# Kernel tuning notes

Hardware: AMD Instinct MI355X
Metric: run time of the kernel (lower is better)

## Reference

```python
import jax, jax.numpy as jnp
import numpy as np
from jax import lax
from jax.scipy.linalg import cho_solve, solve_triangular

N_MC, S, O, T, B, M, HL = 16, 4, 3, 128, 256, 32, 64
PAR = S * S + S + S * S  # 36 variational params per timestep
JIT = 1e-5
LOG2PI = float(np.log(2.0 * np.pi))


def _rbf(x, z, inv_ls, os_d):
    # x [..., D], z [M, D] -> [..., M]
    d = (x[..., None, :] - z) * inv_ls
    return os_d * jnp.exp(-0.5 * jnp.sum(d * d, -1))


def setup_inputs():
    key = jax.random.key(0)
    ks = jax.random.split(key, 16)
    r = jax.random.normal
    obs = r(ks[0], (B, T, O), jnp.float32)
    Z = r(ks[1], (S, M, S), jnp.float32)
    log_ls = jnp.zeros((S, S), jnp.float32)
    log_os = jnp.zeros((S,), jnp.float32)
    m_u = 0.1 * r(ks[2], (S, M), jnp.float32)
    L_u = 0.1 * jnp.broadcast_to(jnp.eye(M, dtype=jnp.float32), (S, M, M)) \
        + 0.01 * jnp.tril(r(ks[3], (S, M, M), jnp.float32))
    noise_proc = 0.0025 * jnp.ones((S,), jnp.float32)  # process_noise_sd**2
    noise_emis = 0.01 * jnp.ones((O,), jnp.float32)    # emission_noise_sd**2
    def lin(k, o, i):
        return r(k, (o, i), jnp.float32) / np.sqrt(i).astype(np.float32)
    Wih = lin(ks[4], 4 * HL, O); Whh = lin(ks[5], 4 * HL, HL)
    b_lstm = jnp.zeros((4 * HL,), jnp.float32)
    Wm = lin(ks[6], S, HL); bm = jnp.zeros((S,), jnp.float32)
    Wv = lin(ks[7], S, HL); bv = jnp.zeros((S,), jnp.float32)
    W1 = lin(ks[8], 256, O); b1 = jnp.zeros((256,), jnp.float32)
    W2 = lin(ks[9], 128, 256); b2 = jnp.zeros((128,), jnp.float32)
    W3 = lin(ks[10], 64, 128); b3 = jnp.zeros((64,), jnp.float32)
    W4 = lin(ks[11], PAR, 64); b4 = jnp.zeros((PAR,), jnp.float32)
    return dict(obs=obs, Z=Z, log_ls=log_ls, log_os=log_os, m_u=m_u, L_u=L_u,
                noise_proc=noise_proc, noise_emis=noise_emis,
                Wih=Wih, Whh=Whh, b_lstm=b_lstm, Wm=Wm, bm=bm, Wv=Wv, bv=bv,
                W1=W1, b1=b1, W2=W2, b2=b2, W3=W3, b3=b3, W4=W4, b4=b4)


def reference(obs, Z, log_ls, log_os, m_u, L_u, noise_proc, noise_emis,
              Wih, Whh, b_lstm, Wm, bm, Wv, bv,
              W1, b1, W2, b2, W3, b3, W4, b4):
    ls = jnp.exp(log_ls)                  # [S, S] ARD lengthscales per GP output dim
    os_ = jnp.exp(log_os)                 # [S] outputscales
    inv_ls = 1.0 / ls
    H = jnp.eye(S, dtype=obs.dtype)[:O]   # fixed emission matrix (learn_emission=False)

    # ---- RecNet: LSTM over observations -> q(x0) = N(m0, diag(v0)) ----
    def lstm_cell(carry, x_t):
        h, c = carry
        g = x_t @ Wih.T + h @ Whh.T + b_lstm
        i, f, gg, o = jnp.split(g, 4, -1)
        c = jax.nn.sigmoid(f) * c + jax.nn.sigmoid(i) * jnp.tanh(gg)
        h = jax.nn.sigmoid(o) * jnp.tanh(c)
        return (h, c), None
    h0 = jnp.zeros((B, HL), obs.dtype)
    (hT, _), _ = lax.scan(lstm_cell, (h0, h0), obs.transpose(1, 0, 2))
    m0 = hT @ Wm.T + bm
    v0 = jax.nn.softplus(hT @ Wv.T + bv) + 1e-6
    # KL[q(x0) || N(0, I)]
    qm0_KL = jnp.mean(0.5 * jnp.sum(v0 + m0 ** 2 - 1.0 - jnp.log(v0), -1))

    # ---- sample x0 and inducing outputs U ~ q(u) (consistent sampling) ----
    rng = jax.random.key(42)
    k0, kU, kq = jax.random.split(rng, 3)
    eps0 = jax.random.normal(k0, (N_MC, S, B, S), obs.dtype)
    x_prev = m0 + jnp.sqrt(v0) * eps0     # [N_MC, S, B, S]
    Lu = jnp.tril(L_u)                    # [S, M, M]
    epsU = jax.random.normal(kU, (N_MC, S, M), obs.dtype)
    U = m_u + jnp.einsum('smk,nsk->nsm', Lu, epsU)  # [N_MC, S, M]

    # ---- per-output-dim GP precomputation ----
    Kzz = jax.vmap(lambda z, il, o: _rbf(z, z, il, o))(Z, inv_ls, os_) \
        + JIT * jnp.eye(M, dtype=obs.dtype)
    Lzz = jnp.linalg.cholesky(Kzz)        # [S, M, M]

    def cond_dim(Z_d, inv_ls_d, os_d, Lz_d, U_d, x_d):
        # condition GP dim d on sampled U_d: x_d [N,B,S], U_d [N,M]
        Kxz = _rbf(x_d, Z_d, inv_ls_d, os_d)              # [N,B,M]
        v = cho_solve((Lz_d, True), U_d.T).T              # Kzz^{-1} U, [N,M]
        mean = jnp.einsum('nbm,nm->nb', Kxz, v)
        W_ = cho_solve((Lz_d, True), Kxz.reshape(-1, M).T).T.reshape(N_MC, B, M)
        var = os_d - jnp.sum(Kxz * W_, -1)
        return mean, jnp.maximum(var, 1e-8)
    gp_cond = jax.vmap(cond_dim, in_axes=(0, 0, 0, 0, 1, 1))

    # ---- amortized inference net (4-layer MLP) for all timesteps ----
    h = jax.nn.relu(obs @ W1.T + b1)
    h = jax.nn.relu(h @ W2.T + b2)
    h = jax.nn.relu(h @ W3.T + b3)
    par = h @ W4.T + b4                    # [B, T, PAR]

    eps_q = jax.random.normal(kq, (T, N_MC, B, S), obs.dtype)
    eyeS = jnp.eye(S, dtype=obs.dtype)

    def step(carry, inp):
        x_p, KLa, lika = carry
        par_t, y_t, eps_t = inp            # [B,PAR], [B,O], [N,B,S]
        mean_d, var_d = gp_cond(Z, inv_ls, os_, Lzz, U, x_p)
        gpMean = mean_d.transpose(1, 2, 0)  # [N,B,S]
        gpVar = var_d.transpose(1, 2, 0)
        At = par_t[:, :S * S].reshape(B, S, S)
        bt = par_t[:, S * S:S * S + S]
        Stl = jnp.tril(par_t[:, S * S + S:].reshape(B, S, S))
        St = Stl @ Stl.transpose(0, 2, 1)
        q_mean = jnp.einsum('bij,nbj->nbi', At, gpMean) + bt          # [N,B,S]
        q_cov = St + jnp.einsum('bij,nbj,bkj->nbik', At, gpVar, At)   # [N,B,S,S]
        Lq = jnp.linalg.cholesky(q_cov + 1e-6 * eyeS)
        logdet_q = 2.0 * jnp.sum(jnp.log(jnp.diagonal(Lq, axis1=-2, axis2=-1)), -1)
        d0 = gpVar + noise_proc             # p(xt|ft) diag covariance
        kl_t = 0.5 * (jnp.sum(jnp.diagonal(q_cov, axis1=-2, axis2=-1) / d0, -1)
                      + jnp.sum((gpMean - q_mean) ** 2 / d0, -1)
                      - S + jnp.sum(jnp.log(d0), -1) - logdet_q)
        mu_y = q_mean @ H.T                 # [N,B,O]
        var_y = jnp.einsum('oi,nbij,oj->nbo', H, q_cov, H)
        ell = -0.5 * (LOG2PI + jnp.log(noise_emis)
                      + ((y_t - mu_y) ** 2 + var_y) / noise_emis)
        x_new = q_mean + jnp.einsum('nbij,nbj->nbi', Lq, eps_t)
        x_p = jnp.broadcast_to(x_new[:, None], (N_MC, S, B, S))
        return (x_p, KLa + jnp.mean(kl_t), lika + jnp.mean(jnp.sum(ell, -1))), None

    z0 = jnp.asarray(0.0, obs.dtype)
    (x_p, KL, lik), _ = lax.scan(step, (x_prev, z0, z0),
                                 (par.transpose(1, 0, 2), obs.transpose(1, 0, 2), eps_q))

    # ---- KL[q(u) || p(u)] of the variational GP ----
    A = solve_triangular(Lzz, Lu, lower=True)
    bq = solve_triangular(Lzz, m_u[..., None], lower=True)[..., 0]
    logdetK = 2.0 * jnp.sum(jnp.log(jnp.diagonal(Lzz, axis1=-2, axis2=-1)), -1)
    logdetS = 2.0 * jnp.sum(jnp.log(jnp.abs(jnp.diagonal(Lu, axis1=-2, axis2=-1)) + 1e-12), -1)
    gpKL = 0.5 * jnp.sum(jnp.sum(A ** 2, (-2, -1)) + jnp.sum(bq ** 2, -1)
                         - M + logdetK - logdetS) / (T * B)

    ELBO = -qm0_KL - gpKL + lik - KL
    ELBO = jnp.where(lik > KL, -qm0_KL - gpKL + lik / T - KL, ELBO)
    return ELBO
```

## Files before the change

kernel.cpp:

```cpp
#include <hip/hip_runtime.h>
#include <cstdint>
#include <math.h>

#define NMC   16
#define SDIM  4
#define ODIM  3
#define TLEN  128
#define BDIM  256
#define MDIM  32
#define HLDIM 64
#define PARD  36

#define LOG2PI_F 1.8378770664093453f

typedef float v2f __attribute__((ext_vector_type(2)));
__device__ __forceinline__ v2f v2(float x, float y) { v2f r; r.x = x; r.y = y; return r; }
__device__ __forceinline__ v2f v2s(float x) { return v2(x, x); }
#define PKFMA(a, b, c) __builtin_elementwise_fma((a), (b), (c))

__host__ __device__ inline void threefry2x32(uint32_t k0, uint32_t k1,
                                             uint32_t x0, uint32_t x1,
                                             uint32_t* o0, uint32_t* o1) {
  uint32_t ks0 = k0, ks1 = k1, ks2 = k0 ^ k1 ^ 0x1BD11BDAu;
  x0 += ks0; x1 += ks1;
#define TF_R(r) { x0 += x1; x1 = (x1 << (r)) | (x1 >> (32 - (r))); x1 ^= x0; }
  TF_R(13) TF_R(15) TF_R(26) TF_R(6)  x0 += ks1; x1 += ks2 + 1u;
  TF_R(17) TF_R(29) TF_R(16) TF_R(24) x0 += ks2; x1 += ks0 + 2u;
  TF_R(13) TF_R(15) TF_R(26) TF_R(6)  x0 += ks0; x1 += ks1 + 3u;
  TF_R(17) TF_R(29) TF_R(16) TF_R(24) x0 += ks1; x1 += ks2 + 4u;
  TF_R(13) TF_R(15) TF_R(26) TF_R(6)  x0 += ks2; x1 += ks0 + 5u;
#undef TF_R
  *o0 = x0; *o1 = x1;
}

__device__ inline float erfinv_f32(float x) {
  float w = -log1pf(-x * x);
  float p;
  if (w < 5.0f) {
    w -= 2.5f;
    p = 2.81022636e-08f;
    p = fmaf(p, w, 3.43273939e-07f);
    p = fmaf(p, w, -3.5233877e-06f);
    p = fmaf(p, w, -4.39150654e-06f);
    p = fmaf(p, w, 0.00021858087f);
    p = fmaf(p, w, -0.00125372503f);
    p = fmaf(p, w, -0.00417768164f);
    p = fmaf(p, w, 0.246640727f);
    p = fmaf(p, w, 1.50140941f);
  } else {
    w = sqrtf(w) - 3.0f;
    p = -0.000200214257f;
    p = fmaf(p, w, 0.000100950558f);
    p = fmaf(p, w, 0.00134934322f);
    p = fmaf(p, w, -0.00367342844f);
    p = fmaf(p, w, 0.00573950773f);
    p = fmaf(p, w, -0.0076224613f);
    p = fmaf(p, w, 0.00943887047f);
    p = fmaf(p, w, 1.00167406f);
    p = fmaf(p, w, 2.83297682f);
  }
  return p * x;
}

__device__ inline float bits_to_normal(uint32_t b) {
  float f = __uint_as_float((b >> 9) | 0x3F800000u) - 1.0f;
  const float lo = -0.99999994f;
  float u = f * 2.0f + lo;
  u = fmaxf(lo, u);
  return 1.41421356f * erfinv_f32(u);
}

#define DPP_ROR_ADD(v, ctrl) \
  ((v) + __int_as_float(__builtin_amdgcn_update_dpp(0, __float_as_int(v), (ctrl), 0xf, 0xf, false)))

__device__ __forceinline__ float allred32(float v) {
  v = DPP_ROR_ADD(v, 0x128);
  v = DPP_ROR_ADD(v, 0x124);
  v = DPP_ROR_ADD(v, 0x122);
  v = DPP_ROR_ADD(v, 0x121);
  return v + __shfl_xor(v, 16);
}

__device__ __forceinline__ float sigm_fast(float x) {
  return 1.0f / (1.0f + __expf(-x));
}
__device__ __forceinline__ float tanh_fast(float x) {
  return 1.0f - 2.0f / (1.0f + __expf(2.0f * x));
}


#define MLP_SB 128
__device__ void mlp_part(
    float* smem, const float* __restrict__ obs,
    const float* __restrict__ W1, const float* __restrict__ b1,
    const float* __restrict__ W2, const float* __restrict__ b2,
    const float* __restrict__ W3, const float* __restrict__ b3,
    const float* __restrict__ W4, const float* __restrict__ b4,
    float* __restrict__ par_g) {
  float* xs  = smem;
  float* A_l = smem + 192;
  float* B_l = smem + 192 + 4096;
  const int tid = threadIdx.x;
  const int R0 = blockIdx.x * 64;
  const int tr = tid & 15;
  const int tj = tid >> 4;

  for (int idx = tid; idx < 192; idx += 256) {
    int r = idx & 63, o = idx >> 6;
    xs[o * 64 + r] = obs[(R0 + r) * 3 + o];
  }

  float acc2[4][8];
#pragma unroll
  for (int i = 0; i < 4; ++i)
#pragma unroll
    for (int j = 0; j < 8; ++j) acc2[i][j] = 0.f;

  for (int kc = 0; kc < 4; ++kc) {
    __syncthreads();
    {
      int j = tid & 127, kh = (tid >> 7) * 32;
      const float4* wsrc = (const float4*)(W2 + j * 256 + kc * 64 + kh);
#pragma unroll
      for (int q = 0; q < 8; ++q) {
        float4 v = wsrc[q];
        int k = kh + q * 4;
        B_l[(k + 0) * MLP_SB + j] = v.x;
        B_l[(k + 1) * MLP_SB + j] = v.y;
        B_l[(k + 2) * MLP_SB + j] = v.z;
        B_l[(k + 3) * MLP_SB + j] = v.w;
      }
    }
    {
      int r = tid & 63, q4 = tid >> 6;
      float x0 = xs[r], x1 = xs[64 + r], x2 = xs[128 + r];
      const float4* w1p = (const float4*)(W1 + (kc * 64 + q4 * 16) * 3);
      float4 wv[12];
#pragma unroll
      for (int q = 0; q < 12; ++q) wv[q] = w1p[q];
      const float* wf = (const float*)wv;
#pragma unroll
      for (int i = 0; i < 16; ++i) {
        int k = q4 * 16 + i;
        float v = b1[kc * 64 + k] + wf[i * 3] * x0 + wf[i * 3 + 1] * x1 + wf[i * 3 + 2] * x2;
        A_l[k * 64 + r] = fmaxf(v, 0.f);
      }
    }
    __syncthreads();
    for (int k = 0; k < 64; ++k) {
      float4 av = *(const float4*)&A_l[k * 64 + tr * 4];
      float4 b0 = *(const float4*)&B_l[k * MLP_SB + tj * 8];
      float4 b1v = *(const float4*)&B_l[k * MLP_SB + tj * 8 + 4];
      const float a4[4] = {av.x, av.y, av.z, av.w};
      const float bv8[8] = {b0.x, b0.y, b0.z, b0.w, b1v.x, b1v.y, b1v.z, b1v.w};
#pragma unroll
      for (int ri = 0; ri < 4; ++ri)
#pragma unroll
        for (int ji = 0; ji < 8; ++ji)
          acc2[ri][ji] = fmaf(a4[ri], bv8[ji], acc2[ri][ji]);
    }
  }
  __syncthreads();
#pragma unroll
  for (int ji = 0; ji < 8; ++ji) {
    int j = tj * 8 + ji;
    float bias = b2[j];
    float4 hv;
    hv.x = fmaxf(acc2[0][ji] + bias, 0.f);
    hv.y = fmaxf(acc2[1][ji] + bias, 0.f);
    hv.z = fmaxf(acc2[2][ji] + bias, 0.f);
    hv.w = fmaxf(acc2[3][ji] + bias, 0.f);
    *(float4*)&B_l[j * 64 + tr * 4] = hv;
  }

  float acc3[4][4];
#pragma unroll
  for (int i = 0; i < 4; ++i)
#pragma unroll
    for (int j = 0; j < 4; ++j) acc3[i][j] = 0.f;

  for (int kc = 0; kc < 2; ++kc) {
    __syncthreads();
    {
      int j = tid & 63, kq = (tid >> 6) * 16;
      const float4* wsrc = (const float4*)(W3 + j * 128 + kc * 64 + kq);
#pragma unroll
      for (int q = 0; q < 4; ++q) {
        float4 v = wsrc[q];
        int k = kq + q * 4;
        A_l[(k + 0) * 64 + j] = v.x;
        A_l[(k + 1) * 64 + j] = v.y;
        A_l[(k + 2) * 64 + j] = v.z;
        A_l[(k + 3) * 64 + j] = v.w;
      }
    }
    __syncthreads();
    for (int k = 0; k < 64; ++k) {
      float4 av = *(const float4*)&B_l[(kc * 64 + k) * 64 + tr * 4];
      float4 bv = *(const float4*)&A_l[k * 64 + (tj & 15) * 4];
      const float a4[4] = {av.x, av.y, av.z, av.w};
      const float b4v[4] = {bv.x, bv.y, bv.z, bv.w};
#pragma unroll
      for (int ri = 0; ri < 4; ++ri)
#pragma unroll
        for (int ji = 0; ji < 4; ++ji)
          acc3[ri][ji] = fmaf(a4[ri], b4v[ji], acc3[ri][ji]);
    }
  }
  __syncthreads();
#pragma unroll
  for (int ji = 0; ji < 4; ++ji) {
    int j = tj * 4 + ji;
    float bias = b3[j];
    float4 hv;
    hv.x = fmaxf(acc3[0][ji] + bias, 0.f);
    hv.y = fmaxf(acc3[1][ji] + bias, 0.f);
    hv.z = fmaxf(acc3[2][ji] + bias, 0.f);
    hv.w = fmaxf(acc3[3][ji] + bias, 0.f);
    *(float4*)&A_l[j * 64 + tr * 4] = hv;
  }
  __syncthreads();

  {
    int r = tid & 63;
    int jg = __builtin_amdgcn_readfirstlane(tid >> 6);
    float accp[9];
#pragma unroll
    for (int i = 0; i < 9; ++i) accp[i] = b4[jg * 9 + i];
    for (int k = 0; k < 64; ++k) {
      float hv = A_l[k * 64 + r];
#pragma unroll
      for (int i = 0; i < 9; ++i)
        accp[i] = fmaf(hv, W4[(jg * 9 + i) * 64 + k], accp[i]);
    }
#pragma unroll
    for (int i = 0; i < 9; ++i) par_g[(R0 + r) * 36 + jg * 9 + i] = accp[i];
  }
}

__device__ void lstm_part(
    float* smem, int b, const float* __restrict__ obs,
    const float* __restrict__ Wih, const float* __restrict__ Whh,
    const float* __restrict__ b_lstm,
    const float* __restrict__ Wm, const float* __restrict__ bm,
    const float* __restrict__ Wv, const float* __restrict__ bv,
    float* __restrict__ m0_g, float* __restrict__ v0_g, float* __restrict__ acc) {
  float* g_l = smem;
  float* h_w = smem + 512;
  float* mv_l = smem + 768;
  float* obl = smem + 776;
  const int tid = threadIdx.x;
  const int w = tid >> 6;
  const int l = tid & 63;

  for (int i = tid; i < 384; i += 256) obl[(i / 3) * 4 + (i % 3)] = obs[b * 384 + i];

  float whh_r[64];
  {
    const float4* wsrc = (const float4*)(Whh + tid * 64);
#pragma unroll
    for (int q = 0; q < 16; ++q) {
      float4 v = wsrc[q];
      whh_r[q * 4 + 0] = v.x; whh_r[q * 4 + 1] = v.y;
      whh_r[q * 4 + 2] = v.z; whh_r[q * 4 + 3] = v.w;
    }
  }
  const float wih0 = Wih[tid * 3 + 0];
  const float wih1 = Wih[tid * 3 + 1];
  const float wih2 = Wih[tid * 3 + 2];
  const float bb = b_lstm[tid];

  float c_ = 0.0f;
  h_w[w * 64 + l] = 0.0f;
  __syncthreads();

#pragma unroll 1
  for (int t = 0; t < TLEN; ++t) {
    const float4 xv = *(const float4*)&obl[t * 4];
    const float4* h4 = (const float4*)&h_w[w * 64];
    float a0 = 0.f, a1 = 0.f, a2 = 0.f, a3 = 0.f;
#pragma unroll
    for (int q = 0; q < 16; ++q) {
      float4 hv = h4[q];
      a0 = fmaf(whh_r[q * 4 + 0], hv.x, a0);
      a1 = fmaf(whh_r[q * 4 + 1], hv.y, a1);
      a2 = fmaf(whh_r[q * 4 + 2], hv.z, a2);
      a3 = fmaf(whh_r[q * 4 + 3], hv.w, a3);
    }
    float g = fmaf(wih0, xv.x, fmaf(wih1, xv.y, fmaf(wih2, xv.z, bb))) + ((a0 + a1) + (a2 + a3));
    g_l[((t & 1) * 4 + w) * 64 + l] = g;
    __syncthreads();
    float gi = g_l[((t & 1) * 4 + 0) * 64 + l];
    float gf = g_l[((t & 1) * 4 + 1) * 64 + l];
    float gg = g_l[((t & 1) * 4 + 2) * 64 + l];
    float go = g_l[((t & 1) * 4 + 3) * 64 + l];
    c_ = sigm_fast(gf) * c_ + sigm_fast(gi) * tanh_fast(gg);
    h_w[w * 64 + l] = sigm_fast(go) * tanh_fast(c_);
  }

  if (tid < 8) {
    const int s = tid & 3;
    const bool isv = tid >= 4;
    const float* W = isv ? (Wv + s * 64) : (Wm + s * 64);
    float a = isv ? bv[s] : bm[s];
#pragma unroll
    for (int k = 0; k < 64; ++k) a += W[k] * h_w[k];
    if (!isv) {
      m0_g[b * 4 + s] = a;
      mv_l[s] = a;
    } else {
      float sp = (a > 0.f) ? (a + log1pf(expf(-a))) : log1pf(expf(a));
      float v = sp + 1e-6f;
      v0_g[b * 4 + s] = v;
      mv_l[4 + s] = v;
    }
  }
  if (tid == 0) {
    float s = 0.f;
#pragma unroll
    for (int k = 0; k < 4; ++k) {
      float m = mv_l[k], v = mv_l[4 + k];
      s += 0.5f * (v + m * m - 1.0f - logf(v));
    }
    atomicAdd(&acc[0], s);
  }
}

__device__ void setup_part(
    float* smem, int d, const float* __restrict__ Z,
    const float* __restrict__ log_ls, const float* __restrict__ log_os,
    const float* __restrict__ m_u, const float* __restrict__ L_u,
    uint32_t kUa, uint32_t kUb,
    float* __restrict__ Kinv_g, float* __restrict__ alpha_g, float* __restrict__ acc) {
  float* Kl    = smem;
  float* work  = smem + 1056;
  float* Ul    = smem + 2112;
  float* red   = smem + 2624;
  float* epsUl = smem + 2688;
  const int tid = threadIdx.x;

  {
    int nn7 = tid >> 5, k = tid & 31;
    uint32_t j = (uint32_t)((nn7 * 4 + d) * 32 + k);
    uint32_t o0, o1;
    threefry2x32(kUa, kUb, j, j + 1024u, &o0, &o1);
    epsUl[nn7 * 32 + k] = bits_to_normal(o0);
    epsUl[(nn7 + 8) * 32 + k] = bits_to_normal(o1);
  }

  float il[4];
#pragma unroll
  for (int k = 0; k < 4; ++k) il[k] = expf(-log_ls[d * 4 + k]);
  const float osd = expf(log_os[d]);

  for (int e = tid; e < 1024; e += 256) {
    int i = e >> 5, j = e & 31;
    float s = 0.f;
#pragma unroll
    for (int k = 0; k < 4; ++k) {
      float t_ = (Z[d * 128 + i * 4 + k] - Z[d * 128 + j * 4 + k]) * il[k];
      s += t_ * t_;
    }
    float v = osd * expf(-0.5f * s);
    if (i == j) v += 1e-5f;
    Kl[i * 33 + j] = v;
  }
  __syncthreads();

  for (int jc = 0; jc < 32; ++jc) {
    if (tid == jc) {
      float s = Kl[jc * 33 + jc];
      for (int p = 0; p < jc; ++p) s -= Kl[jc * 33 + p] * Kl[jc * 33 + p];
      Kl[jc * 33 + jc] = sqrtf(s);
    }
    __syncthreads();
    if (tid > jc && tid < 32) {
      float s = Kl[tid * 33 + jc];
      for (int p = 0; p < jc; ++p) s -= Kl[tid * 33 + p] * Kl[jc * 33 + p];
      Kl[tid * 33 + jc] = s / Kl[jc * 33 + jc];
    }
    __syncthreads();
  }

  if (tid < 32) {
    const int col = tid;
    float rdiag[32];
#pragma unroll
    for (int r = 0; r < 32; ++r) rdiag[r] = __builtin_amdgcn_rcpf(Kl[r * 33 + r]);
    float w[32];
#pragma unroll
    for (int r = 0; r < 32; ++r) {
      float s = (r == col) ? 1.f : 0.f;
#pragma unroll
      for (int p = 0; p < 32; ++p)
        if (p < r) s -= Kl[r * 33 + p] * w[p];
      w[r] = s * rdiag[r];
    }
    float w2[32];
#pragma unroll
    for (int rr = 0; rr < 32; ++rr) {
      const int r = 31 - rr;
      float s = w[r];
#pragma unroll
      for (int p = 0; p < 32; ++p)
        if (p > r) s -= Kl[p * 33 + r] * w2[p];
      w2[r] = s * rdiag[r];
    }
#pragma unroll
    for (int r = 0; r < 32; ++r) {
      Kinv_g[(((d >> 1) * 32 + r) * 32 + col) * 2 + (d & 1)] = w2[r];
      work[col * 33 + r] = w2[r];
    }
  }
  for (int e = tid; e < 512; e += 256) {
    int nn = e >> 5, m = e & 31;
    float s = m_u[d * 32 + m];
    for (int k = 0; k <= m; ++k)
      s += L_u[(d * 32 + m) * 32 + k] * epsUl[nn * 32 + k];
    Ul[nn * 32 + m] = s;
  }
  __syncthreads();
  for (int e = tid; e < 512; e += 256) {
    int nn = e >> 5, m = e & 31;
    float s = 0.f;
    for (int mm = 0; mm < 32; ++mm) s += work[mm * 33 + m] * Ul[nn * 32 + mm];
    alpha_g[(d * 16 + nn) * 32 + m] = s;
  }

  float contrib = 0.f;
  if (tid < 32) {
    const int col = tid;
    float rdiag[32];
#pragma unroll
    for (int r = 0; r < 32; ++r) rdiag[r] = __builtin_amdgcn_rcpf(Kl[r * 33 + r]);
    float v[32];
    float sa = 0.f;
#pragma unroll
    for (int r = 0; r < 32; ++r) {
      float lu = L_u[(d * 32 + r) * 32 + col];
      float s = (col <= r) ? lu : 0.f;
#pragma unroll
      for (int p = 0; p < 32; ++p)
        if (p < r) s -= Kl[r * 33 + p] * v[p];
      float vv = s * rdiag[r];
      v[r] = vv;
      sa += vv * vv;
    }
    contrib = sa;
  } else if (tid < 64) {
    float bq[32];
    float sb = 0.f;
#pragma unroll
    for (int r = 0; r < 32; ++r) {
      float s = m_u[d * 32 + r];
#pragma unroll
      for (int p = 0; p < 32; ++p)
        if (p < r) s -= Kl[r * 33 + p] * bq[p];
      float vv = s * __builtin_amdgcn_rcpf(Kl[r * 33 + r]);
      bq[r] = vv;
      sb += vv * vv;
    }
    contrib = (tid == 32) ? sb : 0.f;
  }
  if (tid < 64) red[tid] = contrib;
  __syncthreads();
  if (tid == 0) {
    float s = 0.f;
    for (int i = 0; i < 64; ++i) s += red[i];
    float ldK = 0.f, ldS = 0.f;
    for (int r = 0; r < 32; ++r) {
      ldK += logf(Kl[r * 33 + r]);
      ldS += logf(fabsf(L_u[(d * 32 + r) * 32 + r]) + 1e-12f);
    }
    float g = s - 32.0f + 2.0f * ldK - 2.0f * ldS;
    atomicAdd(&acc[1], 0.5f * g / (128.0f * 256.0f));
  }
}

__global__ __launch_bounds__(256) void prep_kernel(
    const float* obs,
    const float* W1, const float* b1, const float* W2, const float* b2,
    const float* W3, const float* b3, const float* W4, const float* b4,
    const float* Wih, const float* Whh, const float* b_lstm,
    const float* Wm, const float* bm, const float* Wv, const float* bv,
    const float* Z, const float* log_ls, const float* log_os,
    const float* m_u, const float* L_u,
    uint32_t kUa, uint32_t kUb,
    float* par_g, float* m0_g, float* v0_g,
    float* Kinv_g, float* alpha_g, float* acc) {
  __shared__ __align__(16) float smem[12480];
  const int bx = blockIdx.x;
  if (bx < 512) {
    mlp_part(smem, obs, W1, b1, W2, b2, W3, b3, W4, b4, par_g);
  } else if (bx < 768) {
    lstm_part(smem, bx - 512, obs, Wih, Whh, b_lstm, Wm, bm, Wv, bv, m0_g, v0_g, acc);
  } else {
    setup_part(smem, bx - 768, Z, log_ls, log_os, m_u, L_u, kUa, kUb,
               Kinv_g, alpha_g, acc);
  }
}

__global__ __launch_bounds__(256)
__attribute__((amdgpu_waves_per_eu(1, 2)))
void scan_kernel(
    const float* __restrict__ Z, const float* __restrict__ log_ls,
    const float* __restrict__ log_os, const float* __restrict__ noise_proc,
    const float* __restrict__ noise_emis, const float* __restrict__ obs,
    const float* __restrict__ par_g, const float* __restrict__ m0_g,
    const float* __restrict__ v0_g,
    const float* __restrict__ Kinv_g, const float* __restrict__ alpha_g,
    uint32_t k0a, uint32_t k0b, uint32_t kqa, uint32_t kqb,
    float* __restrict__ acc, float* __restrict__ out) {
  __shared__ __align__(16) float parl_raw[32 * 36];
  __shared__ __align__(16) float parl_pk[32 * 40];
  __shared__ __align__(16) float obsl[32 * 4];
  __shared__ __align__(16) float eps0l[8 * 4 * 4];
  __shared__ __align__(16) v2f kbufv[8][2][32];
  __shared__ __align__(16) float epsl[128 * 8 * 4];
  const int tid = threadIdx.x;
  const int c = tid >> 5;
  const int m = tid & 31;
  const int h = c & 1;
  const int cp = c & ~1;
  const int b = blockIdx.x >> 1;
  const int nb = (blockIdx.x & 1) << 3;
  const bool hh = (h != 0);

#pragma unroll
  for (int i = 0; i < 8; ++i) {
    int e = tid + 256 * i;
    int t = e >> 5, cc = (e >> 2) & 7, ss = e & 3;
    uint32_t j = (uint32_t)(((t * 16 + nb + cc) * 256 + b) * 4 + ss);
    uint32_t o0, o1;
    threefry2x32(kqa, kqb, j, j + 1048576u, &o0, &o1);
    epsl[e] = bits_to_normal(o0);
    epsl[((t + 64) * 8 + cc) * 4 + ss] = bits_to_normal(o1);
  }
  if (tid < 128) {
    int cc = tid >> 4, dd = (tid >> 2) & 3, ss = tid & 3;
    uint32_t j = (uint32_t)((((cc * 4 + dd) * 256 + b) * 4) + ss);
    uint32_t o0, o1;
    threefry2x32(k0a, k0b, j, j + 32768u, &o0, &o1);
    eps0l[(cc * 4 + dd) * 4 + ss] = bits_to_normal(nb ? o1 : o0);
  }

  v2f ilp[4], nzp[4], osp;
#pragma unroll
  for (int k = 0; k < 4; ++k) {
    float i0 = expf(-log_ls[(2 * h + 0) * 4 + k]);
    float i1 = expf(-log_ls[(2 * h + 1) * 4 + k]);
    ilp[k] = v2(i0, i1);
    nzp[k] = v2(-Z[(2 * h + 0) * 128 + m * 4 + k] * i0,
                -Z[(2 * h + 1) * 128 + m * 4 + k] * i1);
  }
  osp = v2(expf(log_os[2 * h + 0]), expf(log_os[2 * h + 1]));

  v2f kinv2[32];
  {
    const float4* kg4 = (const float4*)Kinv_g;
#pragma unroll
    for (int q = 0; q < 16; ++q) {
      float4 v = kg4[(h * 32 + m) * 16 + q];
      kinv2[2 * q + 0] = v2(v.x, v.y);
      kinv2[2 * q + 1] = v2(v.z, v.w);
    }
  }
  v2f alrp[2];
#pragma unroll
  for (int cc = 0; cc < 2; ++cc)
    alrp[cc] = v2(alpha_g[((2 * h + 0) * 16 + nb + cp + cc) * 32 + m],
                  alpha_g[((2 * h + 1) * 16 + nb + cp + cc) * 32 + m]);
  float np_[4];
#pragma unroll
  for (int k = 0; k < 4; ++k) np_[k] = noise_proc[k];
  const float ine0 = __builtin_amdgcn_rcpf(noise_emis[0]);
  const float ine1 = __builtin_amdgcn_rcpf(noise_emis[1]);
  const float ine2 = __builtin_amdgcn_rcpf(noise_emis[2]);
  const float cst = 3.0f * LOG2PI_F + logf(noise_emis[0]) + logf(noise_emis[1]) + logf(noise_emis[2]);

  const float4 m0v = *(const float4*)(m0_g + b * 4);
  const float4 v0v = *(const float4*)(v0_g + b * 4);
  const float sq0 = sqrtf(v0v.x), sq1 = sqrtf(v0v.y), sq2 = sqrtf(v0v.z), sq3 = sqrtf(v0v.w);

  __syncthreads();
  v2f kt0[2];
#pragma unroll
  for (int cc = 0; cc < 2; ++cc) {
    const float4 ea = *(const float4*)&eps0l[((cp + cc) * 4 + 2 * h + 0) * 4];
    const float4 eb = *(const float4*)&eps0l[((cp + cc) * 4 + 2 * h + 1) * 4];
    v2f xt0p = v2(fmaf(sq0, ea.x, m0v.x), fmaf(sq0, eb.x, m0v.x));
    v2f xt1p = v2(fmaf(sq1, ea.y, m0v.y), fmaf(sq1, eb.y, m0v.y));
    v2f xt2p = v2(fmaf(sq2, ea.z, m0v.z), fmaf(sq2, eb.z, m0v.z));
    v2f xt3p = v2(fmaf(sq3, ea.w, m0v.w), fmaf(sq3, eb.w, m0v.w));
    v2f d0 = PKFMA(xt0p, ilp[0], nzp[0]);
    v2f d1 = PKFMA(xt1p, ilp[1], nzp[1]);
    v2f d2 = PKFMA(xt2p, ilp[2], nzp[2]);
    v2f d3 = PKFMA(xt3p, ilp[3], nzp[3]);
    v2f ss = PKFMA(d0, d0, PKFMA(d1, d1, PKFMA(d2, d2, d3 * d3)));
    v2f km = osp * v2(__expf(-0.5f * ss.x), __expf(-0.5f * ss.y));
    kt0[cc] = km;
    kbufv[cp + cc][h][m] = km;
  }

  float x0r = 0.f, x1r = 0.f, x2r = 0.f, x3r = 0.f;
  float kl_acc = 0.f, ell_acc = 0.f;

  for (int tc = 0; tc < 4; ++tc) {
    __syncthreads();
    {
      const float4* src = (const float4*)(par_g + (size_t)b * 4608 + tc * 1152);
      float4* dst = (float4*)parl_raw;
      for (int i = tid; i < 288; i += 256) dst[i] = src[i];
      if (tid < 96) obsl[(tid / 3) * 4 + (tid % 3)] = obs[b * 384 + tc * 96 + tid];
    }
    __syncthreads();
    {
      int st = tid >> 3, w = tid & 7;
      const float* r = parl_raw + st * 36;
      float* o = parl_pk + st * 40;
      if (w < 4) {
        o[2 * w + 0] = r[0 * 4 + w]; o[2 * w + 1] = r[1 * 4 + w];
        o[8 + 2 * w + 0] = r[2 * 4 + w]; o[8 + 2 * w + 1] = r[3 * 4 + w];
      } else if (w == 4) {
        o[16] = r[16]; o[17] = r[17]; o[18] = r[18]; o[19] = r[19];
      } else if (w == 5) {
        float l00 = r[20];
        o[20] = l00 * l00;
        o[21] = r[24] * l00;
        o[22] = r[28] * l00;
        o[23] = r[32] * l00;
      } else if (w == 6) {
        o[24] = r[28] * r[24] + r[29] * r[25];
        o[25] = r[32] * r[24] + r[33] * r[25];
        o[28] = r[24] * r[24] + r[25] * r[25];
      } else {
        o[26] = r[28] * r[28] + r[29] * r[29] + r[30] * r[30];
        o[27] = r[32] * r[28] + r[33] * r[29] + r[34] * r[30];
        o[29] = r[32] * r[32] + r[33] * r[33] + r[34] * r[34] + r[35] * r[35];
      }
    }
    __syncthreads();

#pragma unroll 1
    for (int tt = 0; tt < 32; ++tt) {
      const int t = tc * 32 + tt;
      const v2f* pk = (const v2f*)&parl_pk[tt * 40];
      v2f Ac01[4], Ac23[4];
#pragma unroll
      for (int k = 0; k < 4; ++k) { Ac01[k] = pk[k]; Ac23[k] = pk[4 + k]; }
      const v2f bt01 = pk[8], bt23 = pk[9];
      const v2f StA = pk[10];
      const v2f StB = pk[11];
      const v2f StD = pk[12];
      const v2f StE = pk[13];
      const v2f Stx = pk[14];
      const float4 ov = *(const float4*)&obsl[tt * 4];
      const float4 ev = *(const float4*)&epsl[(t * 8 + c) * 4];

      v2f kregp[2];
      if (t != 0) {
        const float xo0 = __shfl_xor(x0r, 32);
        const float xo1 = __shfl_xor(x1r, 32);
        const float xo2 = __shfl_xor(x2r, 32);
        const float xo3 = __shfl_xor(x3r, 32);
#pragma unroll
        for (int cc = 0; cc < 2; ++cc) {
          const bool own = (cc == h);
          float xt0 = own ? x0r : xo0;
          float xt1 = own ? x1r : xo1;
          float xt2 = own ? x2r : xo2;
          float xt3 = own ? x3r : xo3;
          v2f d0 = PKFMA(v2s(xt0), ilp[0], nzp[0]);
          v2f d1 = PKFMA(v2s(xt1), ilp[1], nzp[1]);
          v2f d2 = PKFMA(v2s(xt2), ilp[2], nzp[2]);
          v2f d3 = PKFMA(v2s(xt3), ilp[3], nzp[3]);
          v2f ss = PKFMA(d0, d0, PKFMA(d1, d1, PKFMA(d2, d2, d3 * d3)));
          v2f km = osp * v2(__expf(-0.5f * ss.x), __expf(-0.5f * ss.y));
          kregp[cc] = km;
          kbufv[cp + cc][h][m] = km;
        }
      } else {
        kregp[0] = kt0[0];
        kregp[1] = kt0[1];
      }

      v2f gmloc[2], gvloc[2];
#pragma unroll
      for (int cc = 0; cc < 2; ++cc) {
        const float4* kb4 = (const float4*)&kbufv[cp + cc][h][0];
        v2f aA = v2s(0.f), aB = v2s(0.f);
#pragma unroll
        for (int q = 0; q < 16; ++q) {
          float4 kv = kb4[q];
          aA = PKFMA(kinv2[2 * q + 0], v2(kv.x, kv.y), aA);
          aB = PKFMA(kinv2[2 * q + 1], v2(kv.z, kv.w), aB);
        }
        v2f yp = aA + aB;
        v2f gmp = kregp[cc] * alrp[cc];
        v2f qpp = kregp[cc] * yp;
        gmloc[cc] = v2(allred32(gmp.x), allred32(gmp.y));
        v2f qpr = v2(allred32(qpp.x), allred32(qpp.y));
        gvloc[cc] = __builtin_elementwise_max(osp - qpr, v2s(1e-8f));
      }

      v2f sgm = hh ? gmloc[0] : gmloc[1];
      v2f sgv = hh ? gvloc[0] : gvloc[1];
      v2f rgm = v2(__shfl_xor(sgm.x, 32), __shfl_xor(sgm.y, 32));
      v2f rgv = v2(__shfl_xor(sgv.x, 32), __shfl_xor(sgv.y, 32));
      v2f lgm = hh ? gmloc[1] : gmloc[0];
      v2f lgv = hh ? gvloc[1] : gvloc[0];
      v2f gm01 = hh ? rgm : lgm;
      v2f gm23 = hh ? lgm : rgm;
      v2f gv01 = hh ? rgv : lgv;
      v2f gv23 = hh ? lgv : rgv;
      const float gm0 = gm01.x, gm1 = gm01.y, gm2 = gm23.x, gm3 = gm23.y;
      const float gv0 = gv01.x, gv1 = gv01.y, gv2 = gv23.x, gv3 = gv23.y;

      v2f qm01 = bt01, qm23 = bt23;
      qm01 = PKFMA(Ac01[0], v2s(gm0), qm01);
      qm01 = PKFMA(Ac01[1], v2s(gm1), qm01);
      qm01 = PKFMA(Ac01[2], v2s(gm2), qm01);
      qm01 = PKFMA(Ac01[3], v2s(gm3), qm01);
      qm23 = PKFMA(Ac23[0], v2s(gm0), qm23);
      qm23 = PKFMA(Ac23[1], v2s(gm1), qm23);
      qm23 = PKFMA(Ac23[2], v2s(gm2), qm23);
      qm23 = PKFMA(Ac23[3], v2s(gm3), qm23);

      v2f B01[4], B23[4];
      B01[0] = Ac01[0] * v2s(gv0); B23[0] = Ac23[0] * v2s(gv0);
      B01[1] = Ac01[1] * v2s(gv1); B23[1] = Ac23[1] * v2s(gv1);
      B01[2] = Ac01[2] * v2s(gv2); B23[2] = Ac23[2] * v2s(gv2);
      B01[3] = Ac01[3] * v2s(gv3); B23[3] = Ac23[3] * v2s(gv3);

      v2f c0a = StA, c0b = StB, c1 = StD, c2 = StE;
      float c11 = Stx.x, c33 = Stx.y;
#pragma unroll
      for (int k = 0; k < 4; ++k) {
        float A0k = Ac01[k].x, A1k = Ac01[k].y, A2k = Ac23[k].x, A3k = Ac23[k].y;
        c0a = PKFMA(B01[k], v2s(A0k), c0a);
        c0b = PKFMA(B23[k], v2s(A0k), c0b);
        c1  = PKFMA(B23[k], v2s(A1k), c1);
        c2  = PKFMA(B23[k], v2s(A2k), c2);
        c11 = fmaf(B01[k].y, A1k, c11);
        c33 = fmaf(B23[k].y, A3k, c33);
      }
      const float qc00 = c0a.x, qc10 = c0a.y, qc20 = c0b.x, qc30 = c0b.y;
      const float qc11 = c11, qc21 = c1.x, qc31 = c1.y;
      const float qc22 = c2.x, qc32 = c2.y, qc33 = c33;

      float t00 = qc00 + 1e-6f;
      float i0 = __builtin_amdgcn_rsqf(t00);
      float l00 = t00 * i0;
      float l10 = qc10 * i0, l20 = qc20 * i0, l30 = qc30 * i0;
      float t11 = qc11 + 1e-6f - l10 * l10;
      float i1 = __builtin_amdgcn_rsqf(t11);
      float l11 = t11 * i1;
      float l21 = (qc21 - l20 * l10) * i1;
      float l31 = (qc31 - l30 * l10) * i1;
      float t22 = qc22 + 1e-6f - l20 * l20 - l21 * l21;
      float i2 = __builtin_amdgcn_rsqf(t22);
      float l22 = t22 * i2;
      float l32 = (qc32 - l30 * l20 - l31 * l21) * i2;
      float t33 = qc33 + 1e-6f - l30 * l30 - l31 * l31 - l32 * l32;
      float l33 = t33 * __builtin_amdgcn_rsqf(t33);
      float logdet_q = __logf(t00 * t11 * t22 * t33);

      float dp0 = gv0 + np_[0], dp1 = gv1 + np_[1];
      float dp2 = gv2 + np_[2], dp3 = gv3 + np_[3];
      float rp0 = __builtin_amdgcn_rcpf(dp0), rp1 = __builtin_amdgcn_rcpf(dp1);
      float rp2 = __builtin_amdgcn_rcpf(dp2), rp3 = __builtin_amdgcn_rcpf(dp3);
      v2f e01 = gm01 - qm01, e23 = gm23 - qm23;
      float klsum = (qc00 + e01.x * e01.x) * rp0 + (qc11 + e01.y * e01.y) * rp1 +
                    (qc22 + e23.x * e23.x) * rp2 + (qc33 + e23.y * e23.y) * rp3;
      float kl = 0.5f * (klsum - 4.0f + __logf(dp0 * dp1 * dp2 * dp3) - logdet_q);
      kl_acc += kl;

      float dy0 = ov.x - qm01.x, dy1 = ov.y - qm01.y, dy2 = ov.z - qm23.x;
      float es = -0.5f * (cst + (dy0 * dy0 + qc00) * ine0 +
                          (dy1 * dy1 + qc11) * ine1 + (dy2 * dy2 + qc22) * ine2);
      ell_acc += es;

      x0r = qm01.x + l00 * ev.x;
      x1r = qm01.y + l10 * ev.x + l11 * ev.y;
      x2r = qm23.x + l20 * ev.x + l21 * ev.y + l22 * ev.z;
      x3r = qm23.y + l30 * ev.x + l31 * ev.y + l32 * ev.z + l33 * ev.w;
    }
  }

  if (m == 0) {
    atomicAdd(&acc[2], kl_acc);
    atomicAdd(&acc[3], ell_acc);
  }
  __syncthreads();
  if (tid == 0) {
    __threadfence();
    unsigned prev = atomicAdd((unsigned int*)&acc[8], 1u);
    if (prev == 511u) {
      __threadfence();
      float qm0 = atomicAdd(&acc[0], 0.0f) / 256.0f;
      float gpKL = atomicAdd(&acc[1], 0.0f);
      float KL = atomicAdd(&acc[2], 0.0f) / 4096.0f;
      float lik = atomicAdd(&acc[3], 0.0f) / 4096.0f;
      float e = -qm0 - gpKL + lik - KL;
      if (lik > KL) e = -qm0 - gpKL + lik / 128.0f - KL;
      out[0] = e;
    }
  }
}

extern "C" void kernel_launch(void* const* d_in, const int* in_sizes, int n_in,
                              void* d_out, int out_size, void* d_ws, size_t ws_size,
                              hipStream_t stream) {
  const float* obs        = (const float*)d_in[0];
  const float* Z          = (const float*)d_in[1];
  const float* log_ls     = (const float*)d_in[2];
  const float* log_os     = (const float*)d_in[3];
  const float* m_u        = (const float*)d_in[4];
  const float* L_u        = (const float*)d_in[5];
  const float* noise_proc = (const float*)d_in[6];
  const float* noise_emis = (const float*)d_in[7];
  const float* Wih        = (const float*)d_in[8];
  const float* Whh        = (const float*)d_in[9];
  const float* b_lstm     = (const float*)d_in[10];
  const float* Wm         = (const float*)d_in[11];
  const float* bm         = (const float*)d_in[12];
  const float* Wv         = (const float*)d_in[13];
  const float* bv         = (const float*)d_in[14];
  const float* W1         = (const float*)d_in[15];
  const float* b1         = (const float*)d_in[16];
  const float* W2         = (const float*)d_in[17];
  const float* b2         = (const float*)d_in[18];
  const float* W3         = (const float*)d_in[19];
  const float* b3         = (const float*)d_in[20];
  const float* W4         = (const float*)d_in[21];
  const float* b4         = (const float*)d_in[22];

  float* ws = (float*)d_ws;
  float* m0_g  = ws;
  float* v0_g  = m0_g + 1024;
  float* par_g = v0_g + 1024;
  float* kinvg = par_g + 1179648;
  float* alphg = kinvg + 4096;
  float* accp  = alphg + 2048;

  hipMemsetAsync(accp, 0, 64, stream);

  uint32_t A0, B0, A1, B1, A2, B2;
  threefry2x32(0u, 42u, 0u, 3u, &A0, &B0);
  threefry2x32(0u, 42u, 1u, 4u, &A1, &B1);
  threefry2x32(0u, 42u, 2u, 5u, &A2, &B2);
  const uint32_t k0a = A0, k0b = A1;
  const uint32_t kUa = A2, kUb = B0;
  const uint32_t kqa = B1, kqb = B2;

  prep_kernel<<<772, 256, 0, stream>>>(
      obs, W1, b1, W2, b2, W3, b3, W4, b4,
      Wih, Whh, b_lstm, Wm, bm, Wv, bv,
      Z, log_ls, log_os, m_u, L_u,
      kUa, kUb,
      par_g, m0_g, v0_g, kinvg, alphg, accp);

  scan_kernel<<<512, 256, 0, stream>>>(
      Z, log_ls, log_os, noise_proc, noise_emis, obs,
      par_g, m0_g, v0_g, kinvg, alphg, k0a, k0b, kqa, kqb, accp,
      (float*)d_out);
}
```

Baseline: 552.5 us.

## Exploit Kinv symmetry via rotated diagonal storage to halve quadratic-form FMAs

The quadratic form k^T Kinv k is computed with symmetric rotated storage: each lane keeps 17 diagonals of Kinv (off-diagonals pre-doubled) instead of a full 32-entry row, then multiplies by its own k value. This halves the register footprint and the packed FMAs per timestep in the scan kernel. In exchange, the LDS reads become per-lane rotated scalar v2 loads rather than broadcast float4 loads, which may cause bank conflicts. The setup kernel gains an extra transformation pass with syncs.

```diff
diff --git a/kernel.cpp b/kernel.cpp
--- a/kernel.cpp
+++ b/kernel.cpp
@@ -331,7 +331,7 @@
     const float* __restrict__ log_ls, const float* __restrict__ log_os,
     const float* __restrict__ m_u, const float* __restrict__ L_u,
     uint32_t kUa, uint32_t kUb,
-    float* __restrict__ Kinv_g, float* __restrict__ alpha_g, float* __restrict__ acc) {
+    float* __restrict__ Krot_g, float* __restrict__ alpha_g, float* __restrict__ acc) {
   float* Kl    = smem;
   float* work  = smem + 1056;
   float* Ul    = smem + 2112;
@@ -407,10 +407,7 @@
       w2[r] = s * rdiag[r];
     }
 #pragma unroll
-    for (int r = 0; r < 32; ++r) {
-      Kinv_g[(((d >> 1) * 32 + r) * 32 + col) * 2 + (d & 1)] = w2[r];
-      work[col * 33 + r] = w2[r];
-    }
+    for (int r = 0; r < 32; ++r) work[col * 33 + r] = w2[r];
   }
   for (int e = tid; e < 512; e += 256) {
     int nn = e >> 5, m = e & 31;
@@ -426,6 +423,15 @@
     for (int mm = 0; mm < 32; ++mm) s += work[mm * 33 + m] * Ul[nn * 32 + mm];
     alpha_g[(d * 16 + nn) * 32 + m] = s;
   }
+  __syncthreads();
+
+  for (int e = tid; e < 32 * 17; e += 256) {
+    int mm = e / 17, j = e - mm * 17;
+    int col = (mm + j) & 31;
+    float scale = (j == 0 || j == 16) ? 1.0f : 2.0f;
+    Krot_g[((d >> 1) * 32 + mm) * 34 + j * 2 + (d & 1)] = scale * work[col * 33 + mm];
+  }
+  __syncthreads();
 
   float contrib = 0.f;
   if (tid < 32) {
@@ -487,7 +493,7 @@
     const float* m_u, const float* L_u,
     uint32_t kUa, uint32_t kUb,
     float* par_g, float* m0_g, float* v0_g,
-    float* Kinv_g, float* alpha_g, float* acc) {
+    float* Krot_g, float* alpha_g, float* acc) {
   __shared__ __align__(16) float smem[12480];
   const int bx = blockIdx.x;
   if (bx < 512) {
@@ -496,7 +502,7 @@
     lstm_part(smem, bx - 512, obs, Wih, Whh, b_lstm, Wm, bm, Wv, bv, m0_g, v0_g, acc);
   } else {
     setup_part(smem, bx - 768, Z, log_ls, log_os, m_u, L_u, kUa, kUb,
-               Kinv_g, alpha_g, acc);
+               Krot_g, alpha_g, acc);
   }
 }
 
@@ -508,7 +514,7 @@
     const float* __restrict__ noise_emis, const float* __restrict__ obs,
     const float* __restrict__ par_g, const float* __restrict__ m0_g,
     const float* __restrict__ v0_g,
-    const float* __restrict__ Kinv_g, const float* __restrict__ alpha_g,
+    const float* __restrict__ Krot_g, const float* __restrict__ alpha_g,
     uint32_t k0a, uint32_t k0b, uint32_t kqa, uint32_t kqb,
     float* __restrict__ acc, float* __restrict__ out) {
   __shared__ __align__(16) float parl_raw[32 * 36];
@@ -555,16 +561,16 @@
   }
   osp = v2(expf(log_os[2 * h + 0]), expf(log_os[2 * h + 1]));
 
-  v2f kinv2[32];
+  v2f krot2[17];
   {
-    const float4* kg4 = (const float4*)Kinv_g;
-#pragma unroll
-    for (int q = 0; q < 16; ++q) {
-      float4 v = kg4[(h * 32 + m) * 16 + q];
-      kinv2[2 * q + 0] = v2(v.x, v.y);
-      kinv2[2 * q + 1] = v2(v.z, v.w);
-    }
-  }
+    const v2f* kg2 = (const v2f*)Krot_g;
+#pragma unroll
+    for (int j = 0; j < 17; ++j) krot2[j] = kg2[(h * 32 + m) * 17 + j];
+  }
+  int roff[17];
+#pragma unroll
+  for (int j = 0; j < 17; ++j) roff[j] = (m + j) & 31;
+
   v2f alrp[2];
 #pragma unroll
   for (int cc = 0; cc < 2; ++cc)
@@ -687,17 +693,16 @@
       v2f gmloc[2], gvloc[2];
 #pragma unroll
       for (int cc = 0; cc < 2; ++cc) {
-        const float4* kb4 = (const float4*)&kbufv[cp + cc][h][0];
-        v2f aA = v2s(0.f), aB = v2s(0.f);
-#pragma unroll
-        for (int q = 0; q < 16; ++q) {
-          float4 kv = kb4[q];
-          aA = PKFMA(kinv2[2 * q + 0], v2(kv.x, kv.y), aA);
-          aB = PKFMA(kinv2[2 * q + 1], v2(kv.z, kv.w), aB);
+        const v2f* kb = &kbufv[cp + cc][h][0];
+        v2f aq0 = krot2[0] * kregp[cc];
+        v2f aq1 = v2s(0.f);
+#pragma unroll
+        for (int j = 1; j <= 16; j += 2) {
+          aq0 = PKFMA(krot2[j], kb[roff[j]], aq0);
+          if (j + 1 <= 16) aq1 = PKFMA(krot2[j + 1], kb[roff[j + 1]], aq1);
         }
-        v2f yp = aA + aB;
+        v2f qpp = kregp[cc] * (aq0 + aq1);
         v2f gmp = kregp[cc] * alrp[cc];
-        v2f qpp = kregp[cc] * yp;
         gmloc[cc] = v2(allred32(gmp.x), allred32(gmp.y));
         v2f qpr = v2(allred32(qpp.x), allred32(qpp.y));
         gvloc[cc] = __builtin_elementwise_max(osp - qpr, v2s(1e-8f));
@@ -839,8 +844,8 @@
   float* m0_g  = ws;
   float* v0_g  = m0_g + 1024;
   float* par_g = v0_g + 1024;
-  float* kinvg = par_g + 1179648;
-  float* alphg = kinvg + 4096;
+  float* krotg = par_g + 1179648;
+  float* alphg = krotg + 4096;
   float* accp  = alphg + 2048;
 
   hipMemsetAsync(accp, 0, 64, stream);
@@ -858,10 +863,10 @@
       Wih, Whh, b_lstm, Wm, bm, Wv, bv,
       Z, log_ls, log_os, m_u, L_u,
       kUa, kUb,
-      par_g, m0_g, v0_g, kinvg, alphg, accp);
+      par_g, m0_g, v0_g, krotg, alphg, accp);
 
   scan_kernel<<<512, 256, 0, stream>>>(
       Z, log_ls, log_os, noise_proc, noise_emis, obs,
-      par_g, m0_g, v0_g, kinvg, alphg, k0a, k0b, kqa, kqb, accp,
+      par_g, m0_g, v0_g, krotg, alphg, k0a, k0b, kqa, kqb, accp,
       (float*)d_out);
 }
```

Result: faster. 535.2 us (-3.1%).
